# Kernel tuning notes

Hardware: AMD Instinct MI355X
Metric: run time of the kernel (lower is better)

Reference implementation:

```python
import jax, jax.numpy as jnp
import numpy as np

MOS = 100        # max_output_size
IOU_T = 0.9      # iou_threshold
SCORE_T = 0.9    # score_threshold (sigma=0 -> hard NMS; also subsumes the 0.5 decode threshold)
PRE_NMS = 2048   # top-k candidates kept before greedy NMS (fixed-shape jit-friendly form)


def setup_inputs() -> dict:
    key = jax.random.key(0)
    k1, k2 = jax.random.split(key)
    B, H, W, K = 32, 192, 192, 9
    score_map = jax.random.uniform(k1, (B, H, W, K), dtype=jnp.float32)
    delta_map = jax.random.normal(k2, (B, H, W, 4 * K), dtype=jnp.float32) * 0.1
    # realistic normalized grid anchors: 3 scales x 3 aspect ratios, format (xmin, xmax, ymin, ymax)
    scales = jnp.array([0.05, 0.1, 0.2], jnp.float32)
    ratios = jnp.array([0.5, 1.0, 2.0], jnp.float32)
    ws = (scales[:, None] * jnp.sqrt(ratios)[None, :]).reshape(-1)  # [K]
    hs = (scales[:, None] / jnp.sqrt(ratios)[None, :]).reshape(-1)  # [K]
    cx = ((jnp.arange(W, dtype=jnp.float32) + 0.5) / W)[None, :, None]  # [1,W,1]
    cy = ((jnp.arange(H, dtype=jnp.float32) + 0.5) / H)[:, None, None]  # [H,1,1]
    xmin, xmax, ymin, ymax = jnp.broadcast_arrays(cx - ws / 2, cx + ws / 2, cy - hs / 2, cy + hs / 2)
    anchors = jnp.stack([xmin, xmax, ymin, ymax], axis=-1).astype(jnp.float32)  # [H,W,K,4]
    return {"score_map": score_map, "delta_map": delta_map, "anchors": anchors}


def _decode(anchors, deltas):
    # anchors: [H,W,K,4] (xmin,xmax,ymin,ymax); deltas: [B,H,W,K,4] (tx,ty,tw,th)
    xa = (anchors[..., 0] + anchors[..., 1]) * 0.5
    ya = (anchors[..., 2] + anchors[..., 3]) * 0.5
    wa = anchors[..., 1] - anchors[..., 0]
    ha = anchors[..., 3] - anchors[..., 2]
    tx, ty, tw, th = deltas[..., 0], deltas[..., 1], deltas[..., 2], deltas[..., 3]
    x = tx * wa + xa
    y = ty * ha + ya
    w = jnp.exp(tw) * wa
    h = jnp.exp(th) * ha
    # one-sided clips exactly as in the original
    xmin = jnp.maximum(x - w * 0.5, 0.0)
    xmax = jnp.minimum(x + w * 0.5, 1.0)
    ymin = jnp.maximum(y - h * 0.5, 0.0)
    ymax = jnp.minimum(y + h * 0.5, 1.0)
    # original reorders boxes for tf NMS as (ymax, xmin, ymin, xmax) and returns them in that order
    return jnp.stack([ymax, xmin, ymin, xmax], axis=-1)


def _iou_one_vs_all(box, boxes):
    # box layout: (ymax, xmin, ymin, xmax)
    y2a, x1a, y1a, x2a = box[0], box[1], box[2], box[3]
    y2b, x1b, y1b, x2b = boxes[:, 0], boxes[:, 1], boxes[:, 2], boxes[:, 3]
    area_a = jnp.maximum(y2a - y1a, 0.0) * jnp.maximum(x2a - x1a, 0.0)
    area_b = jnp.maximum(y2b - y1b, 0.0) * jnp.maximum(x2b - x1b, 0.0)
    ih = jnp.maximum(jnp.minimum(y2a, y2b) - jnp.maximum(y1a, y1b), 0.0)
    iw = jnp.maximum(jnp.minimum(x2a, x2b) - jnp.maximum(x1a, x1b), 0.0)
    inter = ih * iw
    return inter / (area_a + area_b - inter + 1e-9)


def _nms_one(scores, boxes):
    # scores: [N], boxes: [N,4]. Hard greedy NMS over top PRE_NMS candidates above SCORE_T.
    masked = jnp.where(scores > SCORE_T, scores, -jnp.inf)
    top_s, top_i = jax.lax.top_k(masked, PRE_NMS)
    top_b = boxes[top_i]  # [PRE_NMS, 4]

    def step(s, _):
        idx = jnp.argmax(s)
        valid = s[idx] > SCORE_T
        box = top_b[idx]
        iou = _iou_one_vs_all(box, top_b)
        s = jnp.where(iou > IOU_T, -jnp.inf, s).at[idx].set(-jnp.inf)
        return s, jnp.where(valid, box, jnp.zeros_like(box))

    _, out = jax.lax.scan(step, top_s, None, length=MOS)
    return out  # [MOS, 4], zero-padded past the last kept box


def reference(score_map, delta_map, anchors):
    B = score_map.shape[0]
    H, W, K = anchors.shape[:3]
    deltas = delta_map.reshape(B, H, W, K, 4)
    boxes = _decode(anchors, deltas).reshape(B, H * W * K, 4)
    scores = score_map.reshape(B, H * W * K)
    return jax.vmap(_nms_one)(scores, boxes)  # [B, MOS, 4]
```

## Files before the change

kernel.cpp:

```cpp
#include <hip/hip_runtime.h>
#include <stdint.h>

#pragma clang fp contract(off)

typedef unsigned long long u64;
typedef unsigned int u32;

#define NH 192
#define NW 192
#define NK 9
#define NPB (NH * NW * NK)
#define PRE_NMS 2048
#define CAP 4096
#define FAST_CAP 512
#define FAST_K 256
#define MOS 100
#define SCORE_T_BITS 0x3F666666u
#define SPEC_BITS   0x3F7E0000u
#define ONE_BITS 0x3F800000u
#define IOU_T 0.9f


__global__ void zero_cnt(int* __restrict__ cnt, int n) {
    int i = threadIdx.x;
    if (i < n) cnt[i] = 0;
}

__global__ void spec_compact_kernel(const uint4* __restrict__ scores,
                                    int* __restrict__ cnt,
                                    u64* __restrict__ keys) {
    __shared__ u64 stage[512];
    __shared__ int lcount, lbase;
    const int t = threadIdx.x;
    if (t == 0) lcount = 0;
    __syncthreads();
    const int b = blockIdx.y;
    const int base_i = blockIdx.x * 4096;
    const uint4* sp = scores + (size_t)b * (NPB / 4) + (size_t)blockIdx.x * 1024;
#pragma unroll
    for (int i = 0; i < 4; ++i) {
        uint4 v = sp[t + i * 256];
        int ei = base_i + (t + i * 256) * 4;
        u32 uu[4] = {v.x, v.y, v.z, v.w};
#pragma unroll
        for (int c = 0; c < 4; ++c) {
            u32 u = uu[c];
            if (u >= SPEC_BITS) {
                int p = atomicAdd(&lcount, 1);
                u32 idx = (u32)(ei + c);
                if (p < 512) stage[p] = ((u64)u << 32) | (u64)(~idx);
            }
        }
    }
    __syncthreads();
    if (t == 0) lbase = atomicAdd(&cnt[b], lcount);
    __syncthreads();
    const int nb = min(lcount, 512), gb = lbase;
    u64* kb = keys + (size_t)b * CAP;
    for (int i = t; i < nb; i += 256) {
        int gp = gb + i;
        if (gp < CAP) kb[gp] = stage[i];
    }
}

__device__ __forceinline__ float4 decode_box(u64 key, int b,
                                             const float4* __restrict__ anchors4,
                                             const float4* __restrict__ deltas4) {
    u32 idx = ~(u32)(key & 0xFFFFFFFFu);
    float4 a = anchors4[idx];
    float4 d = deltas4[(size_t)b * NPB + idx];
    float xa = (a.x + a.y) * 0.5f;
    float ya = (a.z + a.w) * 0.5f;
    float wa = a.y - a.x;
    float ha = a.w - a.z;
    float x = d.x * wa + xa;
    float y = d.y * ha + ya;
    float w = expf(d.z) * wa;
    float h = expf(d.w) * ha;
    float4 bx;
    bx.x = fminf(y + h * 0.5f, 1.f);
    bx.y = fmaxf(x - w * 0.5f, 0.f);
    bx.z = fmaxf(y - h * 0.5f, 0.f);
    bx.w = fminf(x + w * 0.5f, 1.f);
    return bx;
}

__device__ __forceinline__ int wave_nms(const float4* __restrict__ boxes, int n,
                                        float4* __restrict__ out4, int lane) {
    float4 pb0 = make_float4(0.f, 0.f, 0.f, 0.f), pb1 = pb0;
    float pa0 = 0.f, pa1 = 0.f;
    int np = 0;
    if (n <= 0) return 0;
#define ACCEPT(cb, ar) do { \
        if (lane == (np & 63)) { \
            if (np < 64) { pb0 = cb; pa0 = ar; } else { pb1 = cb; pa1 = ar; } \
            out4[np] = cb; } \
        ++np; } while (0)
    float4 n0 = boxes[0];
    float4 n1 = boxes[(1 < n) ? 1 : 0];
    for (int j = 0; j < n; j += 2) {
        const bool have1 = (j + 1 < n);
        float4 c0 = n0, c1 = n1;
        int jn0 = (j + 2 < n) ? j + 2 : j;
        int jn1 = (j + 3 < n) ? j + 3 : jn0;
        n0 = boxes[jn0];
        n1 = boxes[jn1];
        float ar0 = fmaxf(c0.x - c0.z, 0.f) * fmaxf(c0.w - c0.y, 0.f);
        float ar1 = fmaxf(c1.x - c1.z, 0.f) * fmaxf(c1.w - c1.y, 0.f);
        bool s0 = false, s1 = false;
        if (lane < np) {
            float ih = fmaxf(fminf(pb0.x, c0.x) - fmaxf(pb0.z, c0.z), 0.f);
            float iw = fmaxf(fminf(pb0.w, c0.w) - fmaxf(pb0.y, c0.y), 0.f);
            float inter = ih * iw;
            s0 = inter / (pa0 + ar0 - inter + 1e-9f) > IOU_T;
            ih = fmaxf(fminf(pb0.x, c1.x) - fmaxf(pb0.z, c1.z), 0.f);
            iw = fmaxf(fminf(pb0.w, c1.w) - fmaxf(pb0.y, c1.y), 0.f);
            inter = ih * iw;
            s1 = inter / (pa0 + ar1 - inter + 1e-9f) > IOU_T;
        }
        if (lane + 64 < np) {
            float ih = fmaxf(fminf(pb1.x, c0.x) - fmaxf(pb1.z, c0.z), 0.f);
            float iw = fmaxf(fminf(pb1.w, c0.w) - fmaxf(pb1.y, c0.y), 0.f);
            float inter = ih * iw;
            s0 = s0 || (inter / (pa1 + ar0 - inter + 1e-9f) > IOU_T);
            ih = fmaxf(fminf(pb1.x, c1.x) - fmaxf(pb1.z, c1.z), 0.f);
            iw = fmaxf(fminf(pb1.w, c1.w) - fmaxf(pb1.y, c1.y), 0.f);
            inter = ih * iw;
            s1 = s1 || (inter / (pa1 + ar1 - inter + 1e-9f) > IOU_T);
        }
        bool acc0 = !__any(s0);
        bool acc1 = !__any(s1);
        if (acc0) {
            ACCEPT(c0, ar0);
            if (np == MOS) break;
            if (have1 && acc1) {
                float ih = fmaxf(fminf(c0.x, c1.x) - fmaxf(c0.z, c1.z), 0.f);
                float iw = fmaxf(fminf(c0.w, c1.w) - fmaxf(c0.y, c1.y), 0.f);
                float inter = ih * iw;
                if (!(inter / (ar0 + ar1 - inter + 1e-9f) > IOU_T)) {
                    ACCEPT(c1, ar1);
                    if (np == MOS) break;
                }
            }
        } else if (have1 && acc1) {
            ACCEPT(c1, ar1);
            if (np == MOS) break;
        }
    }
#undef ACCEPT
    return np;
}

__global__ __launch_bounds__(256) void sort_nms_kernel(
        const uint4* __restrict__ scores,
        const float* __restrict__ deltas, const float* __restrict__ anchors,
        const int* __restrict__ cnt, const u64* __restrict__ keys,
        float* __restrict__ out) {
    __shared__ __align__(16) u64 key_s[CAP];
    __shared__ __align__(16) float4 boxes[PRE_NMS];
    __shared__ u64 fast_k[FAST_CAP];
    __shared__ int lh[256];
    __shared__ int s_cnt, s_nsel, s_flag, s_cbin, s_sh, s_nc;
    __shared__ u32 s_bd;
    __shared__ int s_tv, s_cumabove, s_skipB;

    const int t = threadIdx.x;
    const int b = blockIdx.x;
    const float4* anchors4 = (const float4*)anchors;
    const float4* deltas4  = (const float4*)deltas;
    float4* out4 = (float4*)out + (size_t)b * MOS;

    const int nc0 = cnt[b];
    const bool valid = (nc0 >= PRE_NMS && nc0 <= CAP);

    if (valid) {
        const u64* kb = keys + (size_t)b * CAP;
#pragma unroll
        for (int p = 0; p < CAP / 256; ++p) {
            int i = t + p * 256;
            key_s[i] = (i < nc0) ? kb[i] : 0ULL;
        }
        if (t == 0) { s_nc = nc0; s_bd = SPEC_BITS; }
        __syncthreads();
    } else {
        const uint4* sp = scores + (size_t)b * (NPB / 4);
        lh[t] = 0;
        __syncthreads();
        for (int i = t; i < NPB / 4; i += 256) {
            uint4 v = sp[i];
            u32 uu[4] = {v.x, v.y, v.z, v.w};
#pragma unroll
            for (int c = 0; c < 4; ++c)
                if (uu[c] > SCORE_T_BITS) atomicAdd(&lh[(uu[c] >> 16) & 0xFF], 1);
        }
        __syncthreads();
        if (t == 0) {
            int cum = 0, tv = -1, cumab = 0;
            for (int v = 255; v >= 0; --v) {
                int h = lh[v];
                if (cum + h >= PRE_NMS) { tv = v; cumab = cum; break; }
                cum += h;
            }
            if (tv < 0) { s_bd = SCORE_T_BITS + 1; s_skipB = 1; }
            else        { s_tv = tv; s_cumabove = cumab; s_skipB = 0; }
        }
        __syncthreads();
        if (!s_skipB) {
            const int tv = s_tv;
            lh[t] = 0;
            __syncthreads();
            for (int i = t; i < NPB / 4; i += 256) {
                uint4 v = sp[i];
                u32 uu[4] = {v.x, v.y, v.z, v.w};
#pragma unroll
                for (int c = 0; c < 4; ++c)
                    if (uu[c] > SCORE_T_BITS && (int)((uu[c] >> 16) & 0xFF) == tv)
                        atomicAdd(&lh[(uu[c] >> 8) & 0xFF], 1);
            }
            __syncthreads();
            if (t == 0) {
                int cum = s_cumabove, iv = 0;
                for (int v = 255; v >= 0; --v) {
                    cum += lh[v];
                    if (cum >= PRE_NMS) {
                        iv = (cum > CAP && v < 255) ? v + 1 : v;
                        break;
                    }
                }
                u32 bd = (((u32)(0x3F00 + tv)) << 16) | ((u32)iv << 8);
                if (bd < SCORE_T_BITS + 1) bd = SCORE_T_BITS + 1;
                s_bd = bd;
            }
        }
        __syncthreads();
        if (t == 0) s_cnt = 0;
        __syncthreads();
        const u32 bd = s_bd;
        for (int i = t; i < NPB / 4; i += 256) {
            uint4 v = sp[i];
            u32 uu[4] = {v.x, v.y, v.z, v.w};
#pragma unroll
            for (int c = 0; c < 4; ++c) {
                if (uu[c] >= bd) {
                    int p = atomicAdd(&s_cnt, 1);
                    u32 idx = (u32)(i * 4 + c);
                    if (p < CAP) key_s[p] = ((u64)uu[c] << 32) | (u64)(~idx);
                }
            }
        }
        __syncthreads();
        if (t == 0) s_nc = min(s_cnt, CAP);
        __syncthreads();
        for (int p = 0; p < CAP / 256; ++p) {
            int i = t + p * 256;
            if (i >= s_nc) key_s[i] = 0ULL;
        }
        __syncthreads();
    }

    const int nc = s_nc;
    if (t == 0) {
        s_cnt = 0;
        u32 dmax = ONE_BITS - s_bd;
        int bits = 32 - __builtin_clz(dmax);
        s_sh = (bits > 8) ? (bits - 8) : 0;
    }
    lh[t] = 0;
    __syncthreads();
    const int sh = s_sh;

#pragma unroll
    for (int p = 0; p < CAP / 256; ++p) {
        int i = t + p * 256;
        if (i < nc) {
            u32 d = ONE_BITS - (u32)(key_s[i] >> 32);
            u32 bin = d >> sh;
            if (bin > 255u) bin = 255u;
            atomicAdd(&lh[bin], 1);
        }
    }
    for (int i = t; i < FAST_CAP; i += 256) fast_k[i] = 0ULL;
    __syncthreads();

    if (t == 0) {
        int cum = 0; bool hit = false;
        for (int v = 0; v < 256; ++v) {
            cum += lh[v];
            if (cum >= FAST_K) {
                if (cum > FAST_CAP) { s_nsel = cum - lh[v]; s_cbin = v - 1; }
                else                { s_nsel = cum;         s_cbin = v; }
                hit = true; break;
            }
        }
        if (!hit) { s_nsel = cum; s_cbin = 255; }
    }
    __syncthreads();
    const int cbin = s_cbin;
    const int n_sel = s_nsel;

#pragma unroll
    for (int p = 0; p < CAP / 256; ++p) {
        int i = t + p * 256;
        if (i < nc) {
            u64 k = key_s[i];
            u32 d = ONE_BITS - (u32)(k >> 32);
            u32 bin = d >> sh;
            if (bin > 255u) bin = 255u;
            if ((int)bin <= cbin) fast_k[atomicAdd(&s_cnt, 1)] = k;
        }
    }
    __syncthreads();

    for (int k = 2; k <= FAST_CAP; k <<= 1) {
        for (int j = k >> 1; j > 0; j >>= 1) {
            for (int i = t; i < FAST_CAP; i += 256) {
                int ix = i ^ j;
                if (ix > i) {
                    u64 a = fast_k[i], c = fast_k[ix];
                    bool up = ((i & k) == 0);
                    if (up ? (a < c) : (a > c)) { fast_k[i] = c; fast_k[ix] = a; }
                }
            }
            __syncthreads();
        }
    }

    for (int i = t; i < FAST_CAP; i += 256)
        boxes[i] = (i < n_sel) ? decode_box(fast_k[i], b, anchors4, deltas4)
                               : make_float4(0.f, 0.f, 0.f, 0.f);
    __syncthreads();

    if (t < 64) {
        int np = wave_nms(boxes, n_sel, out4, t);
        bool success = (np == MOS) || (n_sel == nc);
        if (success)
            for (int i = np + t; i < MOS; i += 64)
                out4[i] = make_float4(0.f, 0.f, 0.f, 0.f);
        if (t == 0) s_flag = success ? 1 : 0;
    }
    __syncthreads();
    if (s_flag) return;

    for (int k = 2; k <= CAP; k <<= 1) {
        for (int j = k >> 1; j > 0; j >>= 1) {
            for (int i = t; i < CAP; i += 256) {
                int ix = i ^ j;
                if (ix > i) {
                    u64 a = key_s[i], c = key_s[ix];
                    bool up = ((i & k) == 0);
                    if (up ? (a < c) : (a > c)) { key_s[i] = c; key_s[ix] = a; }
                }
            }
            __syncthreads();
        }
    }
    const int nvalid = min(nc, PRE_NMS);
    for (int i = t; i < PRE_NMS; i += 256)
        boxes[i] = (i < nvalid) ? decode_box(key_s[i], b, anchors4, deltas4)
                                : make_float4(0.f, 0.f, 0.f, 0.f);
    __syncthreads();
    if (t < 64) {
        int np = wave_nms(boxes, nvalid, out4, t);
        for (int i = np + t; i < MOS; i += 64)
            out4[i] = make_float4(0.f, 0.f, 0.f, 0.f);
    }
}

extern "C" void kernel_launch(void* const* d_in, const int* in_sizes, int n_in,
                              void* d_out, int out_size, void* d_ws, size_t ws_size,
                              hipStream_t stream) {
    const float* score_map = (const float*)d_in[0];
    const float* delta_map = (const float*)d_in[1];
    const float* anchors   = (const float*)d_in[2];
    float* out = (float*)d_out;
    const int B = in_sizes[0] / NPB;

    char* ws = (char*)d_ws;
    int* cnt  = (int*)ws;
    u64* keys = (u64*)(ws + (size_t)B * 4 + 4);
    keys = (u64*)(((uintptr_t)keys + 15) & ~(uintptr_t)15);

    zero_cnt<<<1, 64, 0, stream>>>(cnt, B);
    spec_compact_kernel<<<dim3(NPB / 4096, B), 256, 0, stream>>>(
        (const uint4*)score_map, cnt, keys);
    sort_nms_kernel<<<B, 256, 0, stream>>>(
        (const uint4*)score_map, delta_map, anchors, cnt, keys, out);
}
```

Measured before the change: 297.6 us.

## Use per-block fixed slots for compaction and rank-sort the fast candidates

Each compaction block now writes its candidates to a fixed per-block slot along with its own count. This removes the global atomic counter and the separate zeroing kernel launch. The NMS kernel gathers the slots into shared memory using the per-block counts, and falls back to the full path when any block overflows its slot. The bitonic sort of the 512 fast candidates is replaced by a rank-by-counting scatter, which drops its many barrier phases in exchange for O(n) comparisons per thread.

```diff
diff --git a/kernel.cpp b/kernel.cpp
--- a/kernel.cpp
+++ b/kernel.cpp
@@ -10,6 +10,8 @@
 #define NW 192
 #define NK 9
 #define NPB (NH * NW * NK)
+#define NSLOT 81
+#define SLOT 96
 #define PRE_NMS 2048
 #define CAP 4096
 #define FAST_CAP 512
@@ -21,22 +23,17 @@
 #define IOU_T 0.9f
 
 
-__global__ void zero_cnt(int* __restrict__ cnt, int n) {
-    int i = threadIdx.x;
-    if (i < n) cnt[i] = 0;
-}
-
 __global__ void spec_compact_kernel(const uint4* __restrict__ scores,
-                                    int* __restrict__ cnt,
+                                    int* __restrict__ bcnt,
                                     u64* __restrict__ keys) {
-    __shared__ u64 stage[512];
-    __shared__ int lcount, lbase;
+    __shared__ u64 stage[SLOT];
+    __shared__ int lcount;
     const int t = threadIdx.x;
     if (t == 0) lcount = 0;
     __syncthreads();
-    const int b = blockIdx.y;
-    const int base_i = blockIdx.x * 4096;
-    const uint4* sp = scores + (size_t)b * (NPB / 4) + (size_t)blockIdx.x * 1024;
+    const int b = blockIdx.y, blk = blockIdx.x;
+    const int base_i = blk * 4096;
+    const uint4* sp = scores + (size_t)b * (NPB / 4) + (size_t)blk * 1024;
 #pragma unroll
     for (int i = 0; i < 4; ++i) {
         uint4 v = sp[t + i * 256];
@@ -48,19 +45,16 @@
             if (u >= SPEC_BITS) {
                 int p = atomicAdd(&lcount, 1);
                 u32 idx = (u32)(ei + c);
-                if (p < 512) stage[p] = ((u64)u << 32) | (u64)(~idx);
-            }
-        }
-    }
-    __syncthreads();
-    if (t == 0) lbase = atomicAdd(&cnt[b], lcount);
-    __syncthreads();
-    const int nb = min(lcount, 512), gb = lbase;
-    u64* kb = keys + (size_t)b * CAP;
-    for (int i = t; i < nb; i += 256) {
-        int gp = gb + i;
-        if (gp < CAP) kb[gp] = stage[i];
-    }
+                if (p < SLOT) stage[p] = ((u64)u << 32) | (u64)(~idx);
+            }
+        }
+    }
+    __syncthreads();
+    const int n = lcount;
+    if (t == 0) bcnt[b * NSLOT + blk] = n;
+    u64* kb = keys + ((size_t)b * NSLOT + blk) * SLOT;
+    const int nw = min(n, SLOT);
+    for (int i = t; i < nw; i += 256) kb[i] = stage[i];
 }
 
 __device__ __forceinline__ float4 decode_box(u64 key, int b,
@@ -154,13 +148,14 @@
 __global__ __launch_bounds__(256) void sort_nms_kernel(
         const uint4* __restrict__ scores,
         const float* __restrict__ deltas, const float* __restrict__ anchors,
-        const int* __restrict__ cnt, const u64* __restrict__ keys,
+        const int* __restrict__ bcnt, const u64* __restrict__ keys,
         float* __restrict__ out) {
     __shared__ __align__(16) u64 key_s[CAP];
     __shared__ __align__(16) float4 boxes[PRE_NMS];
     __shared__ u64 fast_k[FAST_CAP];
     __shared__ int lh[256];
-    __shared__ int s_cnt, s_nsel, s_flag, s_cbin, s_sh, s_nc;
+    __shared__ int scnt_s[NSLOT];
+    __shared__ int s_cnt, s_nsel, s_flag, s_cbin, s_sh, s_nc, s_ok;
     __shared__ u32 s_bd;
     __shared__ int s_tv, s_cumabove, s_skipB;
 
@@ -170,17 +165,32 @@
     const float4* deltas4  = (const float4*)deltas;
     float4* out4 = (float4*)out + (size_t)b * MOS;
 
-    const int nc0 = cnt[b];
-    const bool valid = (nc0 >= PRE_NMS && nc0 <= CAP);
-
-    if (valid) {
-        const u64* kb = keys + (size_t)b * CAP;
-#pragma unroll
-        for (int p = 0; p < CAP / 256; ++p) {
-            int i = t + p * 256;
-            key_s[i] = (i < nc0) ? kb[i] : 0ULL;
-        }
-        if (t == 0) { s_nc = nc0; s_bd = SPEC_BITS; }
+    if (t < NSLOT) scnt_s[t] = bcnt[b * NSLOT + t];
+    __syncthreads();
+    if (t == 0) {
+        int total = 0, maxc = 0;
+        for (int s = 0; s < NSLOT; ++s) {
+            int c = scnt_s[s];
+            total += c;
+            maxc = max(maxc, c);
+        }
+        s_nc = total;
+        s_ok = (total >= PRE_NMS && total <= CAP && maxc <= SLOT) ? 1 : 0;
+        s_cnt = 0;
+        s_bd = SPEC_BITS;
+    }
+    __syncthreads();
+
+    if (s_ok) {
+#pragma unroll
+        for (int p = 0; p < CAP / 256; ++p) key_s[t + p * 256] = 0ULL;
+        __syncthreads();
+        const u64* kb = keys + (size_t)b * NSLOT * SLOT;
+        for (int i = t; i < NSLOT * SLOT; i += 256) {
+            int s = i / SLOT, j = i - s * SLOT;
+            if (j < scnt_s[s])
+                key_s[atomicAdd(&s_cnt, 1)] = kb[(size_t)s * SLOT + j];
+        }
         __syncthreads();
     } else {
         const uint4* sp = scores + (size_t)b * (NPB / 4);
@@ -311,23 +321,17 @@
     }
     __syncthreads();
 
-    for (int k = 2; k <= FAST_CAP; k <<= 1) {
-        for (int j = k >> 1; j > 0; j >>= 1) {
-            for (int i = t; i < FAST_CAP; i += 256) {
-                int ix = i ^ j;
-                if (ix > i) {
-                    u64 a = fast_k[i], c = fast_k[ix];
-                    bool up = ((i & k) == 0);
-                    if (up ? (a < c) : (a > c)) { fast_k[i] = c; fast_k[ix] = a; }
-                }
-            }
-            __syncthreads();
-        }
-    }
-
-    for (int i = t; i < FAST_CAP; i += 256)
-        boxes[i] = (i < n_sel) ? decode_box(fast_k[i], b, anchors4, deltas4)
-                               : make_float4(0.f, 0.f, 0.f, 0.f);
+    {
+        u64 k0 = fast_k[t], k1 = fast_k[t + 256];
+        int r0 = 0, r1 = 0;
+        for (int i = 0; i < n_sel; ++i) {
+            u64 kv = fast_k[i];
+            r0 += (kv > k0);
+            r1 += (kv > k1);
+        }
+        if (t < n_sel)       boxes[r0] = decode_box(k0, b, anchors4, deltas4);
+        if (t + 256 < n_sel) boxes[r1] = decode_box(k1, b, anchors4, deltas4);
+    }
     __syncthreads();
 
     if (t < 64) {
@@ -376,13 +380,11 @@
     const int B = in_sizes[0] / NPB;
 
     char* ws = (char*)d_ws;
-    int* cnt  = (int*)ws;
-    u64* keys = (u64*)(ws + (size_t)B * 4 + 4);
-    keys = (u64*)(((uintptr_t)keys + 15) & ~(uintptr_t)15);
-
-    zero_cnt<<<1, 64, 0, stream>>>(cnt, B);
-    spec_compact_kernel<<<dim3(NPB / 4096, B), 256, 0, stream>>>(
-        (const uint4*)score_map, cnt, keys);
+    int* bcnt = (int*)ws;
+    u64* keys = (u64*)(((uintptr_t)(ws + (size_t)B * NSLOT * 4) + 15) & ~(uintptr_t)15);
+
+    spec_compact_kernel<<<dim3(NSLOT, B), 256, 0, stream>>>(
+        (const uint4*)score_map, bcnt, keys);
     sort_nms_kernel<<<B, 256, 0, stream>>>(
-        (const uint4*)score_map, delta_map, anchors, cnt, keys, out);
-}
+        (const uint4*)score_map, delta_map, anchors, bcnt, keys, out);
+}
```

Measured after the change: 277.3 us. 1.07x faster.
